# Kernel optimization log

Measured on AMD Instinct MI355X. Metric: run time of the kernel, lower is better.

Reference implementation:

```python
import jax, jax.numpy as jnp
import numpy as np

T, B, H = 1024, 16, 1024
S = 2048


def setup_inputs() -> dict:
    key = jax.random.key(0)
    k1, k2, k3, k4 = jax.random.split(key, 4)
    output = jax.random.normal(k1, (T, B, H), dtype=jnp.float32)
    memory = jax.random.normal(k2, (S, B, H), dtype=jnp.float32)
    attn_mask = jnp.zeros((B, T, S), dtype=jnp.bool_)  # True = masked
    # linear_out: Linear(2H -> H); torch weight layout [out, in]
    W = jax.random.normal(k3, (H, 2 * H), dtype=jnp.float32) * (1.0 / np.sqrt(2 * H))
    b = jax.random.normal(k4, (H,), dtype=jnp.float32) * 0.01
    return {"output": output, "memory": memory, "attn_mask": attn_mask, "W": W, "b": b}


def reference(output, memory, attn_mask, W, b):
    # scores: (B, T, S) = output^T @ memory (unscaled dot product)
    attn = jnp.einsum('tbh,sbh->bts', output, memory)
    attn = jnp.where(attn_mask, -jnp.inf, attn)
    attn = jax.nn.softmax(attn, axis=2)
    # context: (T, B, H)
    context = jnp.einsum('bts,sbh->tbh', attn, memory)
    combined = jnp.concatenate([context, output], axis=2)  # (T, B, 2H)
    out = jnp.tanh(jnp.einsum('tbd,hd->tbh', combined, W) + b)
    return (out, attn)
```

## Files before the change

kernel.cpp:

```cpp
#include <hip/hip_runtime.h>
#include <hip/hip_bf16.h>
#include <math.h>

#define Tn 1024
#define Bn 16
#define Hn 1024
#define Sn 2048

typedef __attribute__((ext_vector_type(8))) short bf16x8;
typedef __attribute__((ext_vector_type(8))) unsigned short u16x8;
typedef __attribute__((ext_vector_type(4))) float f32x4;

__device__ __forceinline__ unsigned short f2bf(float x) {
  unsigned u = __float_as_uint(x);
  u += 0x7fffu + ((u >> 16) & 1u);
  return (unsigned short)(u >> 16);
}
__device__ __forceinline__ float bf2f(unsigned short h) {
  return __uint_as_float(((unsigned)h) << 16);
}

__device__ __forceinline__ void gload16(const void* g, void* l) {
  __builtin_amdgcn_global_load_lds((const __attribute__((address_space(1))) void*)g,
                                   (__attribute__((address_space(3))) void*)l, 16, 0, 0);
}


__global__ __launch_bounds__(256) void k_split_plane(const float* __restrict__ src,
                                                     unsigned short* __restrict__ hiP,
                                                     unsigned short* __restrict__ loP,
                                                     int rows) {
  const int i = blockIdx.x * 256 + threadIdx.x;
  const int h8 = i & (Hn / 8 - 1);
  const int rem = i >> 7;
  const int b = rem & (Bn - 1);
  const int r = rem >> 4;
  const float4 a = *(const float4*)(src + (size_t)i * 8);
  const float4 c = *(const float4*)(src + (size_t)i * 8 + 4);
  const float v[8] = {a.x, a.y, a.z, a.w, c.x, c.y, c.z, c.w};
  u16x8 hv, lv;
#pragma unroll
  for (int j = 0; j < 8; ++j) {
    const unsigned short h = f2bf(v[j]);
    hv[j] = h;
    lv[j] = f2bf(v[j] - bf2f(h));
  }
  const size_t dst = ((size_t)b * rows + r) * Hn + h8 * 8;
  *(u16x8*)(hiP + dst) = hv;
  *(u16x8*)(loP + dst) = lv;
}

__global__ __launch_bounds__(256) void k_cvt8(const float* __restrict__ src,
                                              unsigned short* __restrict__ dst, int n8) {
  const int i = blockIdx.x * 256 + threadIdx.x;
  if (i >= n8) return;
  const float4 a = *(const float4*)(src + (size_t)i * 8);
  const float4 c = *(const float4*)(src + (size_t)i * 8 + 4);
  u16x8 u;
  u[0] = f2bf(a.x); u[1] = f2bf(a.y); u[2] = f2bf(a.z); u[3] = f2bf(a.w);
  u[4] = f2bf(c.x); u[5] = f2bf(c.y); u[6] = f2bf(c.z); u[7] = f2bf(c.w);
  *(u16x8*)(dst + (size_t)i * 8) = u;
}

__global__ __launch_bounds__(256) void k_trH(const unsigned short* __restrict__ memH,
                                             unsigned short* __restrict__ memT) {
  __shared__ unsigned short L[64 * 72];
  const int t = threadIdx.x;
  const int h0 = blockIdx.x * 64, s0 = blockIdx.y * 64, b = blockIdx.z;
#pragma unroll
  for (int p = 0; p < 2; ++p) {
    const int fid = p * 256 + t;
    const int s_l = fid >> 3;
    const int c = fid & 7;
    const u16x8 v = *(const u16x8*)(memH + ((size_t)b * Sn + s0 + s_l) * Hn + h0 + c * 8);
#pragma unroll
    for (int e = 0; e < 8; ++e) L[(c * 8 + e) * 72 + s_l] = v[e];
  }
  __syncthreads();
#pragma unroll
  for (int p = 0; p < 2; ++p) {
    const int cid = p * 256 + t;
    const int h_l = cid >> 3;
    const int c = cid & 7;
    const u16x8 vv = *(const u16x8*)&L[h_l * 72 + c * 8];
    *(u16x8*)(memT + ((size_t)b * Hn + h0 + h_l) * Sn + s0 + c * 8) = vv;
  }
}


__device__ __forceinline__ void stage128x32(const unsigned short* __restrict__ g, size_t ldr,
                                            unsigned short* __restrict__ lds, int tid) {
  const int wv = tid >> 6;
  const int row = tid >> 2;
  const size_t coff = (size_t)(tid & 3) * 8;
#pragma unroll
  for (int q = 0; q < 2; ++q)
    gload16(g + (size_t)(q * 64 + row) * ldr + coff, lds + q * 2048 + wv * 512);
}

__device__ __forceinline__ void stage128x64(const unsigned short* __restrict__ g, size_t ldr,
                                            unsigned short* __restrict__ lds, int tid) {
  const int wv = tid >> 6;
  const int row = tid >> 3;
  const size_t coff = (size_t)(tid & 7) * 8;
#pragma unroll
  for (int q = 0; q < 4; ++q)
    gload16(g + (size_t)(q * 32 + row) * ldr + coff, lds + q * 2048 + wv * 512);
}


__global__ __launch_bounds__(256, 3) void k_scores(const unsigned short* __restrict__ oH,
                                                   const unsigned short* __restrict__ oL,
                                                   const unsigned short* __restrict__ mH,
                                                   const unsigned short* __restrict__ mL,
                                                   float* __restrict__ attn) {
  __shared__ unsigned short AsH[128 * 32], AsL[128 * 32], BsH[128 * 32], BsL[128 * 32];
  const int tid = threadIdx.x, lane = tid & 63, wv = tid >> 6;
  const int wm = (wv >> 1) * 64, wn = (wv & 1) * 64;
  const int bs = blockIdx.x * 128, bt = blockIdx.y * 128, b = blockIdx.z;
  const f32x4 fz = {0.f, 0.f, 0.f, 0.f};
  f32x4 acc[4][4];
#pragma unroll
  for (int i = 0; i < 4; ++i)
#pragma unroll
    for (int j = 0; j < 4; ++j) acc[i][j] = fz;

  const unsigned short* AgH = oH + ((size_t)b * Tn + bt) * Hn;
  const unsigned short* AgL = oL + ((size_t)b * Tn + bt) * Hn;
  const unsigned short* BgH = mH + ((size_t)b * Sn + bs) * Hn;
  const unsigned short* BgL = mL + ((size_t)b * Sn + bs) * Hn;
  const int r16 = lane & 15, kh = (lane >> 4) * 8;
  for (int k0 = 0; k0 < Hn; k0 += 32) {
    stage128x32(AgH + k0, Hn, AsH, tid);
    stage128x32(AgL + k0, Hn, AsL, tid);
    stage128x32(BgH + k0, Hn, BsH, tid);
    stage128x32(BgL + k0, Hn, BsL, tid);
    __syncthreads();
    bf16x8 ah[4], al[4];
#pragma unroll
    for (int i = 0; i < 4; ++i) {
      ah[i] = *(const bf16x8*)&AsH[(wm + i * 16 + r16) * 32 + kh];
      al[i] = *(const bf16x8*)&AsL[(wm + i * 16 + r16) * 32 + kh];
    }
#pragma unroll
    for (int j = 0; j < 4; ++j) {
      const bf16x8 bh = *(const bf16x8*)&BsH[(wn + j * 16 + r16) * 32 + kh];
      const bf16x8 bl = *(const bf16x8*)&BsL[(wn + j * 16 + r16) * 32 + kh];
#pragma unroll
      for (int i = 0; i < 4; ++i) {
        acc[i][j] = __builtin_amdgcn_mfma_f32_16x16x32_bf16(ah[i], bh, acc[i][j], 0, 0, 0);
        acc[i][j] = __builtin_amdgcn_mfma_f32_16x16x32_bf16(ah[i], bl, acc[i][j], 0, 0, 0);
        acc[i][j] = __builtin_amdgcn_mfma_f32_16x16x32_bf16(al[i], bh, acc[i][j], 0, 0, 0);
      }
    }
    __syncthreads();
  }
  const int rq = (lane >> 4) * 4;
  float* obase = attn + (size_t)b * Tn * Sn;
#pragma unroll
  for (int i = 0; i < 4; ++i)
#pragma unroll
    for (int q = 0; q < 4; ++q) {
      const int t = bt + wm + i * 16 + rq + q;
#pragma unroll
      for (int j = 0; j < 4; ++j) {
        const int s = bs + wn + j * 16 + r16;
        obase[(size_t)t * Sn + s] = acc[i][j][q];
      }
    }
}


__global__ __launch_bounds__(256) void k_softmax(float* __restrict__ attn,
                                                 const unsigned char* __restrict__ mask,
                                                 unsigned short* __restrict__ attnbf) {
  const int row = blockIdx.x;
  float* p = attn + (size_t)row * Sn;
  const unsigned char* mrow = mask + (size_t)row * Sn;
  const int tid = threadIdx.x;
  const int lane = tid & 63;
  const int wv = tid >> 6;
  const float4 a = *(const float4*)(p + tid * 8);
  const float4 c = *(const float4*)(p + tid * 8 + 4);
  const unsigned long long mv = *(const unsigned long long*)(mrow + tid * 8);
  float x[8] = {a.x, a.y, a.z, a.w, c.x, c.y, c.z, c.w};
#pragma unroll
  for (int j = 0; j < 8; ++j)
    if ((mv >> (8 * j)) & 0xffull) x[j] = -INFINITY;
  float mx = x[0];
#pragma unroll
  for (int j = 1; j < 8; ++j) mx = fmaxf(mx, x[j]);
#pragma unroll
  for (int off = 32; off; off >>= 1) mx = fmaxf(mx, __shfl_xor(mx, off, 64));
  __shared__ float redmax[4], redsum[4];
  if (lane == 0) redmax[wv] = mx;
  __syncthreads();
  mx = fmaxf(fmaxf(redmax[0], redmax[1]), fmaxf(redmax[2], redmax[3]));
  float e[8];
  float s = 0.f;
#pragma unroll
  for (int j = 0; j < 8; ++j) {
    e[j] = __expf(x[j] - mx);
    s += e[j];
  }
#pragma unroll
  for (int off = 32; off; off >>= 1) s += __shfl_xor(s, off, 64);
  if (lane == 0) redsum[wv] = s;
  __syncthreads();
  s = redsum[0] + redsum[1] + redsum[2] + redsum[3];
  const float inv = 1.0f / s;
  float o[8];
#pragma unroll
  for (int j = 0; j < 8; ++j) o[j] = e[j] * inv;
  float4 o0 = {o[0], o[1], o[2], o[3]};
  float4 o1 = {o[4], o[5], o[6], o[7]};
  *(float4*)(p + tid * 8) = o0;
  *(float4*)(p + tid * 8 + 4) = o1;
  u16x8 ub;
#pragma unroll
  for (int j = 0; j < 8; ++j) ub[j] = f2bf(o[j]);
  *(u16x8*)(attnbf + (size_t)row * Sn + tid * 8) = ub;
}


__device__ __forceinline__ void mfma64(const unsigned short* __restrict__ A,
                                       const unsigned short* __restrict__ B,
                                       int wm, int wn, int lane, f32x4 (&acc)[4][4]) {
  const int r16 = lane & 15;
  const int kh = (lane >> 4) * 8;
#pragma unroll
  for (int ks = 0; ks < 2; ++ks) {
    bf16x8 a[4], bb[4];
#pragma unroll
    for (int i = 0; i < 4; ++i) a[i] = *(const bf16x8*)&A[(wm + i * 16 + r16) * 64 + ks * 32 + kh];
#pragma unroll
    for (int j = 0; j < 4; ++j) bb[j] = *(const bf16x8*)&B[(wn + j * 16 + r16) * 64 + ks * 32 + kh];
#pragma unroll
    for (int i = 0; i < 4; ++i)
#pragma unroll
      for (int j = 0; j < 4; ++j)
        acc[i][j] = __builtin_amdgcn_mfma_f32_16x16x32_bf16(a[i], bb[j], acc[i][j], 0, 0, 0);
  }
}

__global__ __launch_bounds__(256, 3) void k_context(const unsigned short* __restrict__ attnbf,
                                                    const unsigned short* __restrict__ memT,
                                                    unsigned short* __restrict__ ctxB) {
  __shared__ unsigned short As[128 * 64], Bs[128 * 64];
  const int tid = threadIdx.x, lane = tid & 63, wv = tid >> 6;
  const int wm = (wv >> 1) * 64, wn = (wv & 1) * 64;
  const int bh = blockIdx.x * 128, bt = blockIdx.y * 128, b = blockIdx.z;
  const f32x4 fz = {0.f, 0.f, 0.f, 0.f};
  f32x4 acc[4][4];
#pragma unroll
  for (int i = 0; i < 4; ++i)
#pragma unroll
    for (int j = 0; j < 4; ++j) acc[i][j] = fz;

  const unsigned short* Ag = attnbf + ((size_t)b * Tn + bt) * Sn;
  const unsigned short* Bg = memT + ((size_t)b * Hn + bh) * Sn;
  for (int k0 = 0; k0 < Sn; k0 += 64) {
    stage128x64(Ag + k0, Sn, As, tid);
    stage128x64(Bg + k0, Sn, Bs, tid);
    __syncthreads();
    mfma64(As, Bs, wm, wn, lane, acc);
    __syncthreads();
  }
  const int r16 = lane & 15, rq = (lane >> 4) * 4;
#pragma unroll
  for (int i = 0; i < 4; ++i)
#pragma unroll
    for (int q = 0; q < 4; ++q) {
      const int t = bt + wm + i * 16 + rq + q;
#pragma unroll
      for (int j = 0; j < 4; ++j) {
        const int h = bh + wn + j * 16 + r16;
        ctxB[((size_t)b * Tn + t) * Hn + h] = f2bf(acc[i][j][q]);
      }
    }
}

__global__ __launch_bounds__(256, 3) void k_final(const unsigned short* __restrict__ ctxB,
                                                  const unsigned short* __restrict__ outpH,
                                                  const unsigned short* __restrict__ Wbf,
                                                  const float* __restrict__ bias,
                                                  float* __restrict__ out) {
  __shared__ unsigned short As[128 * 64], Bs[128 * 64];
  const int tid = threadIdx.x, lane = tid & 63, wv = tid >> 6;
  const int wm = (wv >> 1) * 64, wn = (wv & 1) * 64;
  const int bh = blockIdx.x * 128, bm = blockIdx.y * 128;
  const f32x4 fz = {0.f, 0.f, 0.f, 0.f};
  f32x4 acc[4][4];
#pragma unroll
  for (int i = 0; i < 4; ++i)
#pragma unroll
    for (int j = 0; j < 4; ++j) acc[i][j] = fz;

  for (int k0 = 0; k0 < 2 * Hn; k0 += 64) {
    const unsigned short* Ag = (k0 < Hn) ? (ctxB + (size_t)bm * Hn + k0)
                                         : (outpH + (size_t)bm * Hn + (k0 - Hn));
    stage128x64(Ag, Hn, As, tid);
    stage128x64(Wbf + (size_t)bh * (2 * Hn) + k0, 2 * Hn, Bs, tid);
    __syncthreads();
    mfma64(As, Bs, wm, wn, lane, acc);
    __syncthreads();
  }
  const int r16 = lane & 15, rq = (lane >> 4) * 4;
  float bj[4];
#pragma unroll
  for (int j = 0; j < 4; ++j) bj[j] = bias[bh + wn + j * 16 + r16];
#pragma unroll
  for (int i = 0; i < 4; ++i)
#pragma unroll
    for (int q = 0; q < 4; ++q) {
      const int r = bm + wm + i * 16 + rq + q;
      const int b = r >> 10, t = r & (Tn - 1);
#pragma unroll
      for (int j = 0; j < 4; ++j) {
        const int h = bh + wn + j * 16 + r16;
        out[((size_t)t * Bn + b) * Hn + h] = tanhf(acc[i][j][q] + bj[j]);
      }
    }
}

extern "C" void kernel_launch(void* const* d_in, const int* in_sizes, int n_in,
                              void* d_out, int out_size, void* d_ws, size_t ws_size,
                              hipStream_t stream) {
  const float* outp = (const float*)d_in[0];
  const float* mem = (const float*)d_in[1];
  const unsigned char* mask = (const unsigned char*)d_in[2];
  const float* W = (const float*)d_in[3];
  const float* bias = (const float*)d_in[4];
  float* out = (float*)d_out;
  float* attn = out + (size_t)Tn * Bn * Hn;

  char* w = (char*)d_ws;
  unsigned short* memH  = (unsigned short*)(w);
  unsigned short* memL  = (unsigned short*)(w + ((size_t)64 << 20));
  unsigned short* outpH = (unsigned short*)(w + ((size_t)128 << 20));
  unsigned short* outpL = (unsigned short*)(w + ((size_t)160 << 20));
  unsigned short* Wbf   = (unsigned short*)(w + ((size_t)192 << 20));
  unsigned short* memT   = memL;
  unsigned short* attnbf = memH;
  unsigned short* ctxB   = outpL;

  k_split_plane<<<dim3((Tn * Bn * Hn / 8) / 256), 256, 0, stream>>>(outp, outpH, outpL, Tn);
  k_split_plane<<<dim3((Sn * Bn * Hn / 8) / 256), 256, 0, stream>>>(mem, memH, memL, Sn);
  k_cvt8<<<dim3((Hn * 2 * Hn / 8) / 256), 256, 0, stream>>>(W, Wbf, Hn * 2 * Hn / 8);

  k_scores<<<dim3(Sn / 128, Tn / 128, Bn), 256, 0, stream>>>(outpH, outpL, memH, memL, attn);
  k_trH<<<dim3(Hn / 64, Sn / 64, Bn), 256, 0, stream>>>(memH, memT);
  k_softmax<<<dim3(Bn * Tn), 256, 0, stream>>>(attn, mask, attnbf);
  k_context<<<dim3(Hn / 128, Tn / 128, Bn), 256, 0, stream>>>(attnbf, memT, ctxB);
  k_final<<<dim3(Hn / 128, (Tn * Bn) / 128), 256, 0, stream>>>(ctxB, outpH, Wbf, bias, out);
}
```

Baseline: 565.9 us.

## Double-buffer LDS tiles in scores, context and final GEMM kernels

Converts the three MFMA GEMM kernels to a two-stage LDS ping-pong. Each iteration issues the global_load_lds prefetch of the next K tile before running the MFMAs on the current tile, which removes one barrier per iteration and is meant to overlap global memory latency with compute. LDS per block doubles, so launch bounds drop from 3 to 2 blocks per CU. That trades occupancy for overlap.

```diff
diff --git a/kernel.cpp b/kernel.cpp
--- a/kernel.cpp
+++ b/kernel.cpp
@@ -109,12 +109,13 @@
 }
 
 
-__global__ __launch_bounds__(256, 3) void k_scores(const unsigned short* __restrict__ oH,
+__global__ __launch_bounds__(256, 2) void k_scores(const unsigned short* __restrict__ oH,
                                                    const unsigned short* __restrict__ oL,
                                                    const unsigned short* __restrict__ mH,
                                                    const unsigned short* __restrict__ mL,
                                                    float* __restrict__ attn) {
-  __shared__ unsigned short AsH[128 * 32], AsL[128 * 32], BsH[128 * 32], BsL[128 * 32];
+  __shared__ unsigned short AsH[2][128 * 32], AsL[2][128 * 32];
+  __shared__ unsigned short BsH[2][128 * 32], BsL[2][128 * 32];
   const int tid = threadIdx.x, lane = tid & 63, wv = tid >> 6;
   const int wm = (wv >> 1) * 64, wn = (wv & 1) * 64;
   const int bs = blockIdx.x * 128, bt = blockIdx.y * 128, b = blockIdx.z;
@@ -130,22 +131,38 @@
   const unsigned short* BgH = mH + ((size_t)b * Sn + bs) * Hn;
   const unsigned short* BgL = mL + ((size_t)b * Sn + bs) * Hn;
   const int r16 = lane & 15, kh = (lane >> 4) * 8;
-  for (int k0 = 0; k0 < Hn; k0 += 32) {
-    stage128x32(AgH + k0, Hn, AsH, tid);
-    stage128x32(AgL + k0, Hn, AsL, tid);
-    stage128x32(BgH + k0, Hn, BsH, tid);
-    stage128x32(BgL + k0, Hn, BsL, tid);
-    __syncthreads();
+  const int NK = Hn / 32;
+
+  stage128x32(AgH, Hn, AsH[0], tid);
+  stage128x32(AgL, Hn, AsL[0], tid);
+  stage128x32(BgH, Hn, BsH[0], tid);
+  stage128x32(BgL, Hn, BsL[0], tid);
+  __syncthreads();
+
+#pragma unroll 2
+  for (int t = 0; t < NK; ++t) {
+    const int cur = t & 1;
+    if (t + 1 < NK) {
+      const int k0 = (t + 1) * 32;
+      stage128x32(AgH + k0, Hn, AsH[cur ^ 1], tid);
+      stage128x32(AgL + k0, Hn, AsL[cur ^ 1], tid);
+      stage128x32(BgH + k0, Hn, BsH[cur ^ 1], tid);
+      stage128x32(BgL + k0, Hn, BsL[cur ^ 1], tid);
+    }
+    const unsigned short* AH = AsH[cur];
+    const unsigned short* AL = AsL[cur];
+    const unsigned short* BH = BsH[cur];
+    const unsigned short* BL = BsL[cur];
     bf16x8 ah[4], al[4];
 #pragma unroll
     for (int i = 0; i < 4; ++i) {
-      ah[i] = *(const bf16x8*)&AsH[(wm + i * 16 + r16) * 32 + kh];
-      al[i] = *(const bf16x8*)&AsL[(wm + i * 16 + r16) * 32 + kh];
+      ah[i] = *(const bf16x8*)&AH[(wm + i * 16 + r16) * 32 + kh];
+      al[i] = *(const bf16x8*)&AL[(wm + i * 16 + r16) * 32 + kh];
     }
 #pragma unroll
     for (int j = 0; j < 4; ++j) {
-      const bf16x8 bh = *(const bf16x8*)&BsH[(wn + j * 16 + r16) * 32 + kh];
-      const bf16x8 bl = *(const bf16x8*)&BsL[(wn + j * 16 + r16) * 32 + kh];
+      const bf16x8 bh = *(const bf16x8*)&BH[(wn + j * 16 + r16) * 32 + kh];
+      const bf16x8 bl = *(const bf16x8*)&BL[(wn + j * 16 + r16) * 32 + kh];
 #pragma unroll
       for (int i = 0; i < 4; ++i) {
         acc[i][j] = __builtin_amdgcn_mfma_f32_16x16x32_bf16(ah[i], bh, acc[i][j], 0, 0, 0);
@@ -243,10 +260,10 @@
   }
 }
 
-__global__ __launch_bounds__(256, 3) void k_context(const unsigned short* __restrict__ attnbf,
+__global__ __launch_bounds__(256, 2) void k_context(const unsigned short* __restrict__ attnbf,
                                                     const unsigned short* __restrict__ memT,
                                                     unsigned short* __restrict__ ctxB) {
-  __shared__ unsigned short As[128 * 64], Bs[128 * 64];
+  __shared__ unsigned short As[2][128 * 64], Bs[2][128 * 64];
   const int tid = threadIdx.x, lane = tid & 63, wv = tid >> 6;
   const int wm = (wv >> 1) * 64, wn = (wv & 1) * 64;
   const int bh = blockIdx.x * 128, bt = blockIdx.y * 128, b = blockIdx.z;
@@ -259,11 +276,19 @@
 
   const unsigned short* Ag = attnbf + ((size_t)b * Tn + bt) * Sn;
   const unsigned short* Bg = memT + ((size_t)b * Hn + bh) * Sn;
-  for (int k0 = 0; k0 < Sn; k0 += 64) {
-    stage128x64(Ag + k0, Sn, As, tid);
-    stage128x64(Bg + k0, Sn, Bs, tid);
-    __syncthreads();
-    mfma64(As, Bs, wm, wn, lane, acc);
+  const int NK = Sn / 64;
+  stage128x64(Ag, Sn, As[0], tid);
+  stage128x64(Bg, Sn, Bs[0], tid);
+  __syncthreads();
+#pragma unroll 2
+  for (int t = 0; t < NK; ++t) {
+    const int cur = t & 1;
+    if (t + 1 < NK) {
+      const int k0 = (t + 1) * 64;
+      stage128x64(Ag + k0, Sn, As[cur ^ 1], tid);
+      stage128x64(Bg + k0, Sn, Bs[cur ^ 1], tid);
+    }
+    mfma64(As[cur], Bs[cur], wm, wn, lane, acc);
     __syncthreads();
   }
   const int r16 = lane & 15, rq = (lane >> 4) * 4;
@@ -280,12 +305,12 @@
     }
 }
 
-__global__ __launch_bounds__(256, 3) void k_final(const unsigned short* __restrict__ ctxB,
+__global__ __launch_bounds__(256, 2) void k_final(const unsigned short* __restrict__ ctxB,
                                                   const unsigned short* __restrict__ outpH,
                                                   const unsigned short* __restrict__ Wbf,
                                                   const float* __restrict__ bias,
                                                   float* __restrict__ out) {
-  __shared__ unsigned short As[128 * 64], Bs[128 * 64];
+  __shared__ unsigned short As[2][128 * 64], Bs[2][128 * 64];
   const int tid = threadIdx.x, lane = tid & 63, wv = tid >> 6;
   const int wm = (wv >> 1) * 64, wn = (wv & 1) * 64;
   const int bh = blockIdx.x * 128, bm = blockIdx.y * 128;
@@ -296,13 +321,22 @@
 #pragma unroll
     for (int j = 0; j < 4; ++j) acc[i][j] = fz;
 
-  for (int k0 = 0; k0 < 2 * Hn; k0 += 64) {
-    const unsigned short* Ag = (k0 < Hn) ? (ctxB + (size_t)bm * Hn + k0)
-                                         : (outpH + (size_t)bm * Hn + (k0 - Hn));
-    stage128x64(Ag, Hn, As, tid);
-    stage128x64(Wbf + (size_t)bh * (2 * Hn) + k0, 2 * Hn, Bs, tid);
-    __syncthreads();
-    mfma64(As, Bs, wm, wn, lane, acc);
+  const int NK = (2 * Hn) / 64;
+  auto Asrc = [&](int t) -> const unsigned short* {
+    const int k0 = t * 64;
+    return (k0 < Hn) ? (ctxB + (size_t)bm * Hn + k0) : (outpH + (size_t)bm * Hn + (k0 - Hn));
+  };
+  stage128x64(Asrc(0), Hn, As[0], tid);
+  stage128x64(Wbf + (size_t)bh * (2 * Hn), 2 * Hn, Bs[0], tid);
+  __syncthreads();
+#pragma unroll 2
+  for (int t = 0; t < NK; ++t) {
+    const int cur = t & 1;
+    if (t + 1 < NK) {
+      stage128x64(Asrc(t + 1), Hn, As[cur ^ 1], tid);
+      stage128x64(Wbf + (size_t)bh * (2 * Hn) + (t + 1) * 64, 2 * Hn, Bs[cur ^ 1], tid);
+    }
+    mfma64(As[cur], Bs[cur], wm, wn, lane, acc);
     __syncthreads();
   }
   const int r16 = lane & 15, rq = (lane >> 4) * 4;
```

Measured after the change: 618.1 us. 1.09x slower.
